# Optimization experiments

Measured on AMD Instinct MI355X. Metric: run time of the kernel, lower is better.

Reference implementation:

```python
import jax, jax.numpy as jnp
import numpy as np

B, S, HID = 1, 2048, 3584
NUM_HEADS, KV_HEADS, HEAD_DIM = 28, 4, 128
MROPE = [16, 24, 24]
HEAVY_RATIO, RECENT_RATIO, SINK, MIN_SEQ = 0.1, 0.1, 4, 1024
SCALING = HEAD_DIM ** -0.5
ROPE_THETA = 1000000.0


def rotate_half(x):
    h = x.shape[-1] // 2
    return jnp.concatenate([-x[..., h:], x[..., :h]], axis=-1)


def apply_mrope(q, k, cos, sin, mrope_section):
    # cos/sin: [3, B, S, head_dim]; interleave sections from the 3 position axes
    sec = mrope_section * 2
    splits = list(np.cumsum(sec)[:-1])
    cos_m = jnp.concatenate([m[i % 3] for i, m in enumerate(jnp.split(cos, splits, axis=-1))], axis=-1)[:, None]  # [B,1,S,D]
    sin_m = jnp.concatenate([m[i % 3] for i, m in enumerate(jnp.split(sin, splits, axis=-1))], axis=-1)[:, None]
    q_emb = q * cos_m + rotate_half(q) * sin_m
    k_emb = k * cos_m + rotate_half(k) * sin_m
    return q_emb, k_emb


def h2o_keep_mask(attn_weights, kv_len):
    # attn_weights: [B, H, Q, KV] post-softmax; accumulated score per head/key
    scores = attn_weights.sum(axis=(0, 2))  # [H, KV]
    heavy = max(1, int(HEAVY_RATIO * kv_len))
    recent = max(1, int(RECENT_RATIO * kv_len))
    keep = jnp.zeros((NUM_HEADS, kv_len), dtype=bool)
    ips = max(SINK * 2, int(0.2 * kv_len))  # image-protect prefix
    if kv_len > 3 * ips:
        keep = keep.at[:, :ips].set(True)
        ms = ips
    else:
        keep = keep.at[:, :SINK].set(True)
        ms = SINK
    keep = keep.at[:, kv_len - recent:].set(True)
    me = kv_len - recent
    k = min(heavy, me - ms)
    _, idx = jax.lax.top_k(scores[:, ms:me], k)  # [H, k]
    keep = keep.at[jnp.arange(NUM_HEADS)[:, None], idx + ms].set(True)
    return keep[None, :, None, :]  # [1, H, 1, KV]


def setup_inputs() -> dict:
    key = jax.random.key(0)
    ks = jax.random.split(key, 8)
    hidden_states = jax.random.normal(ks[0], (B, S, HID), jnp.float32)
    # additive causal mask
    causal = jnp.triu(jnp.full((S, S), -1e9, jnp.float32), k=1)
    attention_mask = causal[None, None]
    # mrope cos/sin (same positions on all 3 axes for text-only prefill)
    inv_freq = 1.0 / (ROPE_THETA ** (jnp.arange(0, HEAD_DIM, 2, dtype=jnp.float32) / HEAD_DIM))
    pos = jnp.arange(S, dtype=jnp.float32)
    freqs = pos[:, None] * inv_freq[None, :]            # [S, D/2]
    emb = jnp.concatenate([freqs, freqs], axis=-1)      # [S, D]
    cos = jnp.broadcast_to(jnp.cos(emb)[None, None], (3, B, S, HEAD_DIM))
    sin = jnp.broadcast_to(jnp.sin(emb)[None, None], (3, B, S, HEAD_DIM))
    sd = 0.02
    q_w = jax.random.normal(ks[1], (NUM_HEADS * HEAD_DIM, HID), jnp.float32) * sd
    q_b = jax.random.normal(ks[2], (NUM_HEADS * HEAD_DIM,), jnp.float32) * sd
    k_w = jax.random.normal(ks[3], (KV_HEADS * HEAD_DIM, HID), jnp.float32) * sd
    k_b = jax.random.normal(ks[4], (KV_HEADS * HEAD_DIM,), jnp.float32) * sd
    v_w = jax.random.normal(ks[5], (KV_HEADS * HEAD_DIM, HID), jnp.float32) * sd
    v_b = jax.random.normal(ks[6], (KV_HEADS * HEAD_DIM,), jnp.float32) * sd
    o_w = jax.random.normal(ks[7], (HID, NUM_HEADS * HEAD_DIM), jnp.float32) * sd
    return {"hidden_states": hidden_states, "attention_mask": attention_mask, "cos": cos, "sin": sin,
            "q_w": q_w, "q_b": q_b, "k_w": k_w, "k_b": k_b, "v_w": v_w, "v_b": v_b, "o_w": o_w}


def reference(hidden_states, attention_mask, cos, sin, q_w, q_b, k_w, k_b, v_w, v_b, o_w):
    b, s, _ = hidden_states.shape
    q = (hidden_states @ q_w.T + q_b).reshape(b, s, NUM_HEADS, HEAD_DIM).transpose(0, 2, 1, 3)
    k = (hidden_states @ k_w.T + k_b).reshape(b, s, KV_HEADS, HEAD_DIM).transpose(0, 2, 1, 3)
    v = (hidden_states @ v_w.T + v_b).reshape(b, s, KV_HEADS, HEAD_DIM).transpose(0, 2, 1, 3)
    q, k = apply_mrope(q, k, cos, sin, MROPE)
    n_rep = NUM_HEADS // KV_HEADS
    k = jnp.repeat(k, n_rep, axis=1)  # matches torch repeat_kv layout
    v = jnp.repeat(v, n_rep, axis=1)
    aw = jnp.einsum('bhqd,bhkd->bhqk', q, k) * SCALING + attention_mask
    aw = jax.nn.softmax(aw.astype(jnp.float32), axis=-1).astype(q.dtype)
    kv_len = s
    heavy = max(1, int(HEAVY_RATIO * kv_len))
    recent = max(1, int(RECENT_RATIO * kv_len))
    if kv_len >= MIN_SEQ and kv_len > SINK + recent + heavy:
        mask = h2o_keep_mask(jax.lax.stop_gradient(aw), kv_len)
        aw = aw * mask.astype(aw.dtype)
        aw = aw / jnp.clip(aw.sum(-1, keepdims=True), 1e-9)
    out = jnp.einsum('bhqk,bhkd->bhqd', aw, v)
    out = out.transpose(0, 2, 1, 3).reshape(b, s, NUM_HEADS * HEAD_DIM)
    return out @ o_w.T
```

## Files before the change

### kernel.cpp

```cpp
#include <hip/hip_runtime.h>
#include <hip/hip_bf16.h>
#include <stdint.h>

#define S_LEN 2048
#define HID 3584
#define NHEADS 28
#define KVHEADS 4
#define HD 128
#define QKV_N 4608
#define NREP 7
#define SCALE 0.08838834764831845f
#define NJOBS 896
#define NJOBS_LS 448

typedef __attribute__((ext_vector_type(8))) short bf16x8;
typedef __attribute__((ext_vector_type(8))) _Float16 f16x8;
typedef __attribute__((ext_vector_type(4))) float f32x4;

#define MFMA_B16(a, b, c) __builtin_amdgcn_mfma_f32_16x16x32_bf16((a), (b), (c), 0, 0, 0)
#define MFMA_F16(a, b, c) __builtin_amdgcn_mfma_f32_16x16x32_f16((a), (b), (c), 0, 0, 0)

__device__ __forceinline__ void gl_lds16(const void* g, void* l) {
  __builtin_amdgcn_global_load_lds(
      (__attribute__((address_space(1))) void*)(void*)(g),
      (__attribute__((address_space(3))) void*)(l), 16, 0, 0);
}

__global__ void cvt_f32_f16(const float* __restrict__ src, _Float16* __restrict__ dst, int n4) {
  int i = blockIdx.x * 256 + threadIdx.x;
  if (i >= n4) return;
  float4 v = ((const float4*)src)[i];
  _Float16 t[4] = {(_Float16)v.x, (_Float16)v.y, (_Float16)v.z, (_Float16)v.w};
  ((uint2*)dst)[i] = *(const uint2*)t;
}

template <bool HAS_BIAS>
__global__ __launch_bounds__(256, 4) void gemm_f16(
    const _Float16* __restrict__ A, int lda,
    const _Float16* __restrict__ B, int ldb,
    const float* __restrict__ bias, float* __restrict__ C, int ldc, int K) {
  __shared__ _Float16 lA[128 * 64], lB[128 * 64];
  const int tid = threadIdx.x;
  const int lane = tid & 63;
  const int wid = tid >> 6;
  const int wr = wid >> 1, wc = wid & 1;
  const int l15 = lane & 15, l4 = lane >> 4;
  const int bm = blockIdx.y * 128, bn = blockIdx.x * 128;
  f32x4 acc[4][4] = {};
  for (int k0 = 0; k0 < K; k0 += 64) {
    __syncthreads();
#pragma unroll
    for (int it = 0; it < 4; ++it) {
      int c = it * 256 + tid;
      int rw = c >> 3, sl = c & 7;
      int gcol = (sl ^ (rw & 7)) << 3;
      int lo = (it * 256 + (tid & 192)) * 8;
      gl_lds16(A + (size_t)(bm + rw) * lda + (k0 + gcol), &lA[lo]);
      gl_lds16(B + (size_t)(bn + rw) * ldb + (k0 + gcol), &lB[lo]);
    }
    __syncthreads();
#pragma unroll
    for (int kk = 0; kk < 2; ++kk) {
      f16x8 af[4], bf[4];
#pragma unroll
      for (int m = 0; m < 4; ++m) {
        int rA = wr * 64 + m * 16 + l15;
        af[m] = *(const f16x8*)&lA[rA * 64 + (((kk * 4 + l4) ^ (rA & 7)) << 3)];
      }
#pragma unroll
      for (int n = 0; n < 4; ++n) {
        int rB = wc * 64 + n * 16 + l15;
        bf[n] = *(const f16x8*)&lB[rB * 64 + (((kk * 4 + l4) ^ (rB & 7)) << 3)];
      }
#pragma unroll
      for (int m = 0; m < 4; ++m)
#pragma unroll
        for (int n = 0; n < 4; ++n)
          acc[m][n] = MFMA_F16(af[m], bf[n], acc[m][n]);
    }
  }
#pragma unroll
  for (int m = 0; m < 4; ++m)
#pragma unroll
    for (int n = 0; n < 4; ++n)
#pragma unroll
      for (int r = 0; r < 4; ++r) {
        size_t row = bm + wr * 64 + m * 16 + l4 * 4 + r;
        size_t col = bn + wc * 64 + n * 16 + l15;
        float v = acc[m][n][r];
        if (HAS_BIAS) v += bias[col];
        C[row * ldc + col] = v;
      }
}

__global__ void rope_f16(const float* __restrict__ qf, const float* __restrict__ cb,
                         const float* __restrict__ sb,
                         _Float16* __restrict__ q16, _Float16* __restrict__ k16) {
  int idx = blockIdx.x * 256 + threadIdx.x;
  int d1 = idx & 63;
  int hh = (idx >> 6) & 31;
  int s = idx >> 11;
  if (s >= S_LEN) return;
  const float* row = qf + (size_t)s * QKV_N + (hh < NHEADS ? hh * HD : HID + (hh - NHEADS) * HD);
  int d2 = d1 + 64;
  int ax1 = (d1 < 32) ? 0 : 1;
  int ax2 = (d2 < 80) ? 1 : 2;
  float c1 = cb[(size_t)ax1 * S_LEN * HD + (size_t)s * HD + d1];
  float s1 = sb[(size_t)ax1 * S_LEN * HD + (size_t)s * HD + d1];
  float c2 = cb[(size_t)ax2 * S_LEN * HD + (size_t)s * HD + d2];
  float s2 = sb[(size_t)ax2 * S_LEN * HD + (size_t)s * HD + d2];
  float x1 = row[d1], x2 = row[d2];
  float y1 = x1 * c1 - x2 * s1;
  float y2 = x2 * c2 + x1 * s2;
  _Float16* dp;
  size_t base;
  if (hh < NHEADS) { dp = q16; base = (size_t)s * HID + hh * HD; }
  else { dp = k16; base = (size_t)s * 512 + (hh - NHEADS) * HD; }
  dp[base + d1] = (_Float16)y1;
  dp[base + d2] = (_Float16)y2;
}

__global__ void vtrans(const float* __restrict__ qf, __hip_bfloat16* __restrict__ vt) {
  __shared__ __hip_bfloat16 t[64][65];
  const int j = blockIdx.z;
  const int d0 = blockIdx.y * 64;
  const int k0 = blockIdx.x * 64;
  const int tid = threadIdx.x;
#pragma unroll
  for (int half = 0; half < 2; ++half) {
    int r = half * 32 + (tid >> 3);
    int c = (tid & 7) * 8;
    const float* p = qf + (size_t)(k0 + r) * QKV_N + (HID + 512) + j * HD + d0 + c;
    float4 a = ((const float4*)p)[0];
    float4 b = ((const float4*)p)[1];
    t[c + 0][r] = __float2bfloat16(a.x); t[c + 1][r] = __float2bfloat16(a.y);
    t[c + 2][r] = __float2bfloat16(a.z); t[c + 3][r] = __float2bfloat16(a.w);
    t[c + 4][r] = __float2bfloat16(b.x); t[c + 5][r] = __float2bfloat16(b.y);
    t[c + 6][r] = __float2bfloat16(b.z); t[c + 7][r] = __float2bfloat16(b.w);
  }
  __syncthreads();
#pragma unroll
  for (int half = 0; half < 2; ++half) {
    int r = half * 32 + (tid >> 3);
    int c = (tid & 7) * 8;
    __hip_bfloat16 tmp[8];
#pragma unroll
    for (int u = 0; u < 8; ++u) tmp[u] = t[r][c + u];
    *(bf16x8*)&vt[(size_t)j * (HD * S_LEN) + (size_t)(d0 + r) * S_LEN + k0 + c] = *(const bf16x8*)tmp;
  }
}

template <typename T>
__device__ __forceinline__ void stageK_sw(T* dst, const T* gsrc, int ldg, int tid) {
#pragma unroll
  for (int it = 0; it < 4; ++it) {
    int c = it * 256 + tid;
    int rw = c >> 4, sl = c & 15;
    int gcol = (sl ^ (rw & 7)) << 3;
    gl_lds16(gsrc + (size_t)rw * ldg + gcol, dst + (size_t)(it * 256 + (tid & 192)) * 8);
  }
}
__device__ __forceinline__ void stageV_sw(__hip_bfloat16* dst, const __hip_bfloat16* gsrc,
                                          int ldg, int tid) {
#pragma unroll
  for (int it = 0; it < 4; ++it) {
    int c = it * 256 + tid;
    int rw = c >> 3, sl = c & 7;
    int gcol = (sl ^ (rw & 7)) << 3;
    gl_lds16(gsrc + (size_t)rw * ldg + gcol, dst + (size_t)(it * 256 + (tid & 192)) * 8);
  }
}

__global__ __launch_bounds__(256, 4) void attn_ls(
    const _Float16* __restrict__ q16, const _Float16* __restrict__ k16,
    float* __restrict__ scores, int* __restrict__ ctr) {
  __shared__ _Float16 Kh[2][64 * 128];
  __shared__ int sj;
  const int tid = threadIdx.x;
  const int lane = tid & 63, w = tid >> 6;
  const int l15 = lane & 15, l4 = lane >> 4;
  const int sw = l15 & 7;
  for (;;) {
    __syncthreads();
    if (tid == 0) sj = atomicAdd(ctr, 1);
    __syncthreads();
    const int j = sj;
    if (j >= NJOBS_LS) return;
    const int qb = 15 - j / 28, h = j % 28;
    const int hkv = h / NREP;
    const int nt = 2 * qb + 2;
    f16x8 qh[2][4];
#pragma unroll
    for (int f = 0; f < 2; ++f) {
      const _Float16* qp =
          q16 + (size_t)(qb * 128 + w * 32 + f * 16 + l15) * HID + h * HD + l4 * 8;
#pragma unroll
      for (int kk = 0; kk < 4; ++kk) qh[f][kk] = *(const f16x8*)(qp + kk * 32);
    }
    float lsum[2][4] = {};
    stageK_sw(Kh[0], k16 + hkv * HD, 512, tid);
    __syncthreads();
    for (int kt = 0; kt < nt; ++kt) {
      if (kt + 1 < nt)
        stageK_sw(Kh[(kt + 1) & 1], k16 + (size_t)((kt + 1) * 64) * 512 + hkv * HD, 512, tid);
      const _Float16* Kc = Kh[kt & 1];
      f32x4 acc[2][4] = {};
#pragma unroll
      for (int kk = 0; kk < 4; ++kk)
#pragma unroll
        for (int n = 0; n < 4; ++n) {
          f16x8 bh = *(const f16x8*)&Kc[(n * 16 + l15) * 128 + (((kk * 4 + l4) ^ sw) << 3)];
#pragma unroll
          for (int f = 0; f < 2; ++f) acc[f][n] = MFMA_F16(qh[f][kk], bh, acc[f][n]);
        }
      const bool tail = (kt >= 2 * qb);
#pragma unroll
      for (int f = 0; f < 2; ++f)
#pragma unroll
        for (int r = 0; r < 4; ++r) {
          int rowg = qb * 128 + w * 32 + f * 16 + l4 * 4 + r;
#pragma unroll
          for (int n = 0; n < 4; ++n)
            if (!tail || (kt * 64 + n * 16 + l15) <= rowg)
              lsum[f][r] += __expf(acc[f][n][r] * SCALE);
        }
      __syncthreads();
    }
    float invl[2][4];
#pragma unroll
    for (int f = 0; f < 2; ++f)
#pragma unroll
      for (int r = 0; r < 4; ++r) {
        float s = lsum[f][r];
        s += __shfl_xor(s, 1);
        s += __shfl_xor(s, 2);
        s += __shfl_xor(s, 4);
        s += __shfl_xor(s, 8);
        invl[f][r] = 1.0f / s;
      }
    stageK_sw(Kh[0], k16 + hkv * HD, 512, tid);
    __syncthreads();
    for (int kt = 0; kt < nt; ++kt) {
      if (kt + 1 < nt)
        stageK_sw(Kh[(kt + 1) & 1], k16 + (size_t)((kt + 1) * 64) * 512 + hkv * HD, 512, tid);
      const _Float16* Kc = Kh[kt & 1];
      f32x4 acc[2][4] = {};
#pragma unroll
      for (int kk = 0; kk < 4; ++kk)
#pragma unroll
        for (int n = 0; n < 4; ++n) {
          f16x8 bh = *(const f16x8*)&Kc[(n * 16 + l15) * 128 + (((kk * 4 + l4) ^ sw) << 3)];
#pragma unroll
          for (int f = 0; f < 2; ++f) acc[f][n] = MFMA_F16(qh[f][kk], bh, acc[f][n]);
        }
      const bool tail = (kt >= 2 * qb);
      float colsum[4] = {0.f, 0.f, 0.f, 0.f};
#pragma unroll
      for (int f = 0; f < 2; ++f)
#pragma unroll
        for (int r = 0; r < 4; ++r) {
          int rowg = qb * 128 + w * 32 + f * 16 + l4 * 4 + r;
#pragma unroll
          for (int n = 0; n < 4; ++n)
            if (!tail || (kt * 64 + n * 16 + l15) <= rowg)
              colsum[n] += __expf(acc[f][n][r] * SCALE) * invl[f][r];
        }
#pragma unroll
      for (int n = 0; n < 4; ++n) {
        colsum[n] += __shfl_xor(colsum[n], 16);
        colsum[n] += __shfl_xor(colsum[n], 32);
      }
      if (lane < 16) {
#pragma unroll
        for (int n = 0; n < 4; ++n)
          atomicAdd(&scores[h * S_LEN + kt * 64 + n * 16 + lane], colsum[n]);
      }
      __syncthreads();
    }
  }
}

__global__ void h2o_topk(const float* __restrict__ scores, unsigned char* __restrict__ keep) {
  const int h = blockIdx.x;
  const int tid = threadIdx.x;
  const int MS = 409, ME = 1844, REGN = 1435, KSEL = 204;
  __shared__ float sv[1435];
  __shared__ int cnt, eqn;
  __shared__ int eqlist[256];
  for (int i = tid; i < REGN; i += 256) sv[i] = scores[h * S_LEN + MS + i];
  for (int i = tid; i < S_LEN; i += 256)
    keep[h * S_LEN + i] = (i < MS || i >= ME) ? 1 : 0;
  __syncthreads();
  unsigned lo = 0u, hi = 0x7f800000u;
  while (hi - lo > 1u) {
    unsigned mid = lo + ((hi - lo) >> 1);
    if (tid == 0) cnt = 0;
    __syncthreads();
    int lc = 0;
    for (int i = tid; i < REGN; i += 256) lc += (__float_as_uint(sv[i]) >= mid) ? 1 : 0;
    if (lc) atomicAdd(&cnt, lc);
    __syncthreads();
    int c = cnt;
    __syncthreads();
    if (c >= KSEL) lo = mid;
    else hi = mid;
  }
  if (tid == 0) { cnt = 0; eqn = 0; }
  __syncthreads();
  int lgt = 0;
  for (int i = tid; i < REGN; i += 256) {
    unsigned b = __float_as_uint(sv[i]);
    if (b > lo) { keep[h * S_LEN + MS + i] = 1; lgt++; }
    else if (b == lo) {
      int p = atomicAdd(&eqn, 1);
      if (p < 256) eqlist[p] = i;
    }
  }
  if (lgt) atomicAdd(&cnt, lgt);
  __syncthreads();
  if (tid == 0) {
    int r = KSEL - cnt;
    int ne = eqn > 256 ? 256 : eqn;
    for (int t = 0; t < r; ++t) {
      int best = 0x7fffffff, bj = -1;
      for (int j = 0; j < ne; ++j)
        if (eqlist[j] < best) { best = eqlist[j]; bj = j; }
      if (bj < 0) break;
      keep[h * S_LEN + MS + best] = 1;
      eqlist[bj] = 0x7fffffff;
    }
  }
}

__global__ __launch_bounds__(256, 2) void attn_out(
    const _Float16* __restrict__ q16, const _Float16* __restrict__ k16,
    const __hip_bfloat16* __restrict__ vt, const unsigned char* __restrict__ keep,
    _Float16* __restrict__ ctx, int* __restrict__ ctr) {
  __shared__ _Float16 Kh[2][64 * 128];
  __shared__ __hip_bfloat16 Vtl[2][128 * 64];
  __shared__ __hip_bfloat16 Wt[4][16 * 64];
  __shared__ int sj;
  const int tid = threadIdx.x;
  const int lane = tid & 63, w = tid >> 6;
  const int l15 = lane & 15, l4 = lane >> 4;
  const int sw = l15 & 7;
  for (;;) {
    __syncthreads();
    if (tid == 0) sj = atomicAdd(ctr, 1);
    __syncthreads();
    const int j = sj;
    if (j >= NJOBS) return;
    const int qb = 31 - j / 28, h = j % 28;
    const int hkv = h / NREP;
    const int nt = qb + 1;
    f16x8 qh[4];
    {
      const _Float16* qp = q16 + (size_t)(qb * 64 + w * 16 + l15) * HID + h * HD + l4 * 8;
#pragma unroll
      for (int kk = 0; kk < 4; ++kk) qh[kk] = *(const f16x8*)(qp + kk * 32);
    }
    f32x4 o[8] = {};
    float dens[4] = {0.f, 0.f, 0.f, 0.f};
    stageK_sw(Kh[0], k16 + hkv * HD, 512, tid);
    stageV_sw(Vtl[0], vt + (size_t)hkv * (HD * S_LEN), S_LEN, tid);
    __syncthreads();
    for (int kt = 0; kt < nt; ++kt) {
      if (kt + 1 < nt) {
        stageK_sw(Kh[(kt + 1) & 1], k16 + (size_t)((kt + 1) * 64) * 512 + hkv * HD, 512, tid);
        stageV_sw(Vtl[(kt + 1) & 1], vt + (size_t)hkv * (HD * S_LEN) + (kt + 1) * 64, S_LEN, tid);
      }
      const _Float16* Kc = Kh[kt & 1];
      const __hip_bfloat16* Vc = Vtl[kt & 1];
      f32x4 acc[4] = {};
#pragma unroll
      for (int kk = 0; kk < 4; ++kk)
#pragma unroll
        for (int n = 0; n < 4; ++n) {
          f16x8 bh = *(const f16x8*)&Kc[(n * 16 + l15) * 128 + (((kk * 4 + l4) ^ sw) << 3)];
          acc[n] = MFMA_F16(qh[kk], bh, acc[n]);
        }
      const bool diag = (kt == qb);
      float kf[4];
#pragma unroll
      for (int n = 0; n < 4; ++n)
        kf[n] = (float)keep[h * S_LEN + kt * 64 + n * 16 + l15];
#pragma unroll
      for (int r = 0; r < 4; ++r) {
        int rowg = qb * 64 + w * 16 + l4 * 4 + r;
        int row16 = l4 * 4 + r;
#pragma unroll
        for (int n = 0; n < 4; ++n) {
          int coll = n * 16 + l15;
          float wv = 0.f;
          if (!diag || (kt * 64 + coll) <= rowg)
            wv = kf[n] * __expf(acc[n][r] * SCALE);
          dens[r] += wv;
          Wt[w][row16 * 64 + (coll ^ ((row16 & 7) << 3))] = __float2bfloat16(wv);
        }
      }
#pragma unroll
      for (int kk = 0; kk < 2; ++kk) {
        bf16x8 af = *(const bf16x8*)&Wt[w][l15 * 64 + ((kk * 32 + l4 * 8) ^ (sw << 3))];
#pragma unroll
        for (int n = 0; n < 8; ++n) {
          bf16x8 bf = *(const bf16x8*)&Vc[(n * 16 + l15) * 64 + (((kk * 4 + l4) ^ sw) << 3)];
          o[n] = MFMA_B16(af, bf, o[n]);
        }
      }
      __syncthreads();
    }
    float invd[4];
#pragma unroll
    for (int r = 0; r < 4; ++r) {
      float d = dens[r];
      d += __shfl_xor(d, 1);
      d += __shfl_xor(d, 2);
      d += __shfl_xor(d, 4);
      d += __shfl_xor(d, 8);
      invd[r] = 1.0f / fmaxf(d, 1e-30f);
    }
#pragma unroll
    for (int n = 0; n < 8; ++n)
#pragma unroll
      for (int r = 0; r < 4; ++r) {
        size_t row = qb * 64 + w * 16 + l4 * 4 + r;
        size_t col = h * HD + n * 16 + l15;
        ctx[row * HID + col] = (_Float16)(o[n][r] * invd[r]);
      }
  }
}

extern "C" void kernel_launch(void* const* d_in, const int* in_sizes, int n_in,
                              void* d_out, int out_size, void* d_ws, size_t ws_size,
                              hipStream_t stream) {
  const float* hidden = (const float*)d_in[0];
  const float* cosb = (const float*)d_in[2];
  const float* sinb = (const float*)d_in[3];
  const float* q_w = (const float*)d_in[4];
  const float* q_b = (const float*)d_in[5];
  const float* k_w = (const float*)d_in[6];
  const float* k_b = (const float*)d_in[7];
  const float* v_w = (const float*)d_in[8];
  const float* v_b = (const float*)d_in[9];
  const float* o_w = (const float*)d_in[10];

  char* ws = (char*)d_ws;
  float* qkv_f32 = (float*)(ws + 0);
  _Float16* hf16 = (_Float16*)(ws + 37748736);
  _Float16* wqkv16 = (_Float16*)(ws + 52428800);
  float* biasb = (float*)(ws + 85458944);
  _Float16* q16 = (_Float16*)(ws + 37748736);
  _Float16* wo16 = (_Float16*)(ws + 52428800);
  _Float16* k16 = (_Float16*)(ws + 85477376);
  __hip_bfloat16* vt = (__hip_bfloat16*)(ws + 87574528);
  float* scores = (float*)(ws + 89671680);
  unsigned char* keep = (unsigned char*)(ws + 89901056);
  int* ctrs = (int*)(ws + 89958400);
  _Float16* ctx16 = (_Float16*)(ws + 0);

  hipMemcpyAsync(biasb, q_b, 3584 * 4, hipMemcpyDeviceToDevice, stream);
  hipMemcpyAsync(biasb + 3584, k_b, 512 * 4, hipMemcpyDeviceToDevice, stream);
  hipMemcpyAsync(biasb + 4096, v_b, 512 * 4, hipMemcpyDeviceToDevice, stream);

  cvt_f32_f16<<<7168, 256, 0, stream>>>(hidden, hf16, 1835008);
  cvt_f32_f16<<<12544, 256, 0, stream>>>(q_w, wqkv16, 3211264);
  cvt_f32_f16<<<1792, 256, 0, stream>>>(k_w, wqkv16 + (size_t)3584 * 3584, 458752);
  cvt_f32_f16<<<1792, 256, 0, stream>>>(v_w, wqkv16 + (size_t)4096 * 3584, 458752);

  gemm_f16<true><<<dim3(36, 16), 256, 0, stream>>>(hf16, HID, wqkv16, HID,
                                                   biasb, qkv_f32, QKV_N, HID);

  cvt_f32_f16<<<12544, 256, 0, stream>>>(o_w, wo16, 3211264);

  rope_f16<<<16384, 256, 0, stream>>>(qkv_f32, cosb, sinb, q16, k16);
  vtrans<<<dim3(32, 2, 4), 256, 0, stream>>>(qkv_f32, vt);
  hipMemsetAsync(scores, 0, NHEADS * S_LEN * 4, stream);
  hipMemsetAsync(ctrs, 0, 8, stream);

  attn_ls<<<512, 256, 0, stream>>>(q16, k16, scores, &ctrs[0]);
  h2o_topk<<<28, 256, 0, stream>>>(scores, keep);
  attn_out<<<512, 256, 0, stream>>>(q16, k16, vt, keep, ctx16, &ctrs[1]);

  gemm_f16<false><<<dim3(28, 16), 256, 0, stream>>>(ctx16, HID, wo16, HID,
                                                    nullptr, (float*)d_out, HID, HID);
}
```

Baseline: 455.6 us.

## Split H2O score kernel into key-chunked row-sum and column-score passes

The single persistent attn_ls kernel, which computed softmax row sums and then column scores per (query block, head) job, is replaced by two grid-launched kernels. Each splits the key range into chunks of up to eight 64-key tiles, giving 1120 blocks in place of 448 jobs. Row sums are combined with atomics into a new lbuf buffer, and a masking branch is hoisted so full tiles skip the causal check. This aims at better load balance and occupancy for long causal rows, at the cost of an extra launch, more atomics and reloading Q per chunk.

```diff
diff --git a/kernel.cpp b/kernel.cpp
--- a/kernel.cpp
+++ b/kernel.cpp
@@ -11,7 +11,7 @@
 #define NREP 7
 #define SCALE 0.08838834764831845f
 #define NJOBS 896
-#define NJOBS_LS 448
+#define NJOBS_KC 1120
 
 typedef __attribute__((ext_vector_type(8))) short bf16x8;
 typedef __attribute__((ext_vector_type(8))) _Float16 f16x8;
@@ -24,6 +24,13 @@
   __builtin_amdgcn_global_load_lds(
       (__attribute__((address_space(1))) void*)(void*)(g),
       (__attribute__((address_space(3))) void*)(l), 16, 0, 0);
+}
+
+__device__ __forceinline__ void decode_qc(int t, int& qb, int& ck) {
+  if (t < 4) { qb = t; ck = 0; }
+  else if (t < 12) { qb = 4 + ((t - 4) >> 1); ck = (t - 4) & 1; }
+  else if (t < 24) { qb = 8 + (t - 12) / 3; ck = (t - 12) % 3; }
+  else { qb = 12 + ((t - 24) >> 2); ck = (t - 24) & 3; }
 }
 
 __global__ void cvt_f32_f16(const float* __restrict__ src, _Float16* __restrict__ dst, int n4) {
@@ -171,49 +178,55 @@
   }
 }
 
-__global__ __launch_bounds__(256, 4) void attn_ls(
+__global__ __launch_bounds__(256, 4) void attn_l(
     const _Float16* __restrict__ q16, const _Float16* __restrict__ k16,
-    float* __restrict__ scores, int* __restrict__ ctr) {
+    float* __restrict__ lbuf) {
   __shared__ _Float16 Kh[2][64 * 128];
-  __shared__ int sj;
+  const int j = blockIdx.x;
+  const int h = j % 28;
+  int qb, ck;
+  decode_qc(j / 28, qb, ck);
+  const int hkv = h / NREP;
+  const int nt = 2 * qb + 2;
+  const int kt0 = ck * 8;
+  const int kt1 = (kt0 + 8 < nt) ? kt0 + 8 : nt;
   const int tid = threadIdx.x;
   const int lane = tid & 63, w = tid >> 6;
   const int l15 = lane & 15, l4 = lane >> 4;
   const int sw = l15 & 7;
-  for (;;) {
-    __syncthreads();
-    if (tid == 0) sj = atomicAdd(ctr, 1);
-    __syncthreads();
-    const int j = sj;
-    if (j >= NJOBS_LS) return;
-    const int qb = 15 - j / 28, h = j % 28;
-    const int hkv = h / NREP;
-    const int nt = 2 * qb + 2;
-    f16x8 qh[2][4];
-#pragma unroll
-    for (int f = 0; f < 2; ++f) {
-      const _Float16* qp =
-          q16 + (size_t)(qb * 128 + w * 32 + f * 16 + l15) * HID + h * HD + l4 * 8;
-#pragma unroll
-      for (int kk = 0; kk < 4; ++kk) qh[f][kk] = *(const f16x8*)(qp + kk * 32);
-    }
-    float lsum[2][4] = {};
-    stageK_sw(Kh[0], k16 + hkv * HD, 512, tid);
-    __syncthreads();
-    for (int kt = 0; kt < nt; ++kt) {
-      if (kt + 1 < nt)
-        stageK_sw(Kh[(kt + 1) & 1], k16 + (size_t)((kt + 1) * 64) * 512 + hkv * HD, 512, tid);
-      const _Float16* Kc = Kh[kt & 1];
-      f32x4 acc[2][4] = {};
-#pragma unroll
-      for (int kk = 0; kk < 4; ++kk)
-#pragma unroll
-        for (int n = 0; n < 4; ++n) {
-          f16x8 bh = *(const f16x8*)&Kc[(n * 16 + l15) * 128 + (((kk * 4 + l4) ^ sw) << 3)];
-#pragma unroll
-          for (int f = 0; f < 2; ++f) acc[f][n] = MFMA_F16(qh[f][kk], bh, acc[f][n]);
-        }
-      const bool tail = (kt >= 2 * qb);
+  f16x8 qh[2][4];
+#pragma unroll
+  for (int f = 0; f < 2; ++f) {
+    const _Float16* qp =
+        q16 + (size_t)(qb * 128 + w * 32 + f * 16 + l15) * HID + h * HD + l4 * 8;
+#pragma unroll
+    for (int kk = 0; kk < 4; ++kk) qh[f][kk] = *(const f16x8*)(qp + kk * 32);
+  }
+  float lsum[2][4] = {};
+  stageK_sw(Kh[0], k16 + (size_t)(kt0 * 64) * 512 + hkv * HD, 512, tid);
+  __syncthreads();
+  for (int kt = kt0; kt < kt1; ++kt) {
+    if (kt + 1 < kt1)
+      stageK_sw(Kh[(kt + 1) & 1], k16 + (size_t)((kt + 1) * 64) * 512 + hkv * HD, 512, tid);
+    const _Float16* Kc = Kh[kt & 1];
+    f32x4 acc[2][4] = {};
+#pragma unroll
+    for (int kk = 0; kk < 4; ++kk)
+#pragma unroll
+      for (int n = 0; n < 4; ++n) {
+        f16x8 bh = *(const f16x8*)&Kc[(n * 16 + l15) * 128 + (((kk * 4 + l4) ^ sw) << 3)];
+#pragma unroll
+        for (int f = 0; f < 2; ++f) acc[f][n] = MFMA_F16(qh[f][kk], bh, acc[f][n]);
+      }
+    if (kt < 2 * qb) {
+#pragma unroll
+      for (int f = 0; f < 2; ++f)
+#pragma unroll
+        for (int r = 0; r < 4; ++r)
+#pragma unroll
+          for (int n = 0; n < 4; ++n)
+            lsum[f][r] += __expf(acc[f][n][r] * SCALE);
+    } else {
 #pragma unroll
       for (int f = 0; f < 2; ++f)
 #pragma unroll
@@ -221,40 +234,81 @@
           int rowg = qb * 128 + w * 32 + f * 16 + l4 * 4 + r;
 #pragma unroll
           for (int n = 0; n < 4; ++n)
-            if (!tail || (kt * 64 + n * 16 + l15) <= rowg)
+            if ((kt * 64 + n * 16 + l15) <= rowg)
               lsum[f][r] += __expf(acc[f][n][r] * SCALE);
         }
-      __syncthreads();
-    }
-    float invl[2][4];
-#pragma unroll
-    for (int f = 0; f < 2; ++f)
-#pragma unroll
-      for (int r = 0; r < 4; ++r) {
-        float s = lsum[f][r];
-        s += __shfl_xor(s, 1);
-        s += __shfl_xor(s, 2);
-        s += __shfl_xor(s, 4);
-        s += __shfl_xor(s, 8);
-        invl[f][r] = 1.0f / s;
-      }
-    stageK_sw(Kh[0], k16 + hkv * HD, 512, tid);
-    __syncthreads();
-    for (int kt = 0; kt < nt; ++kt) {
-      if (kt + 1 < nt)
-        stageK_sw(Kh[(kt + 1) & 1], k16 + (size_t)((kt + 1) * 64) * 512 + hkv * HD, 512, tid);
-      const _Float16* Kc = Kh[kt & 1];
-      f32x4 acc[2][4] = {};
-#pragma unroll
-      for (int kk = 0; kk < 4; ++kk)
-#pragma unroll
-        for (int n = 0; n < 4; ++n) {
-          f16x8 bh = *(const f16x8*)&Kc[(n * 16 + l15) * 128 + (((kk * 4 + l4) ^ sw) << 3)];
-#pragma unroll
-          for (int f = 0; f < 2; ++f) acc[f][n] = MFMA_F16(qh[f][kk], bh, acc[f][n]);
-        }
-      const bool tail = (kt >= 2 * qb);
-      float colsum[4] = {0.f, 0.f, 0.f, 0.f};
+    }
+    __syncthreads();
+  }
+#pragma unroll
+  for (int f = 0; f < 2; ++f)
+#pragma unroll
+    for (int r = 0; r < 4; ++r) {
+      float s = lsum[f][r];
+      s += __shfl_xor(s, 1);
+      s += __shfl_xor(s, 2);
+      s += __shfl_xor(s, 4);
+      s += __shfl_xor(s, 8);
+      if (l15 == 0)
+        atomicAdd(&lbuf[h * S_LEN + qb * 128 + w * 32 + f * 16 + l4 * 4 + r], s);
+    }
+}
+
+__global__ __launch_bounds__(256, 4) void attn_sc(
+    const _Float16* __restrict__ q16, const _Float16* __restrict__ k16,
+    const float* __restrict__ lbuf, float* __restrict__ scores) {
+  __shared__ _Float16 Kh[2][64 * 128];
+  const int j = blockIdx.x;
+  const int h = j % 28;
+  int qb, ck;
+  decode_qc(j / 28, qb, ck);
+  const int hkv = h / NREP;
+  const int nt = 2 * qb + 2;
+  const int kt0 = ck * 8;
+  const int kt1 = (kt0 + 8 < nt) ? kt0 + 8 : nt;
+  const int tid = threadIdx.x;
+  const int lane = tid & 63, w = tid >> 6;
+  const int l15 = lane & 15, l4 = lane >> 4;
+  const int sw = l15 & 7;
+  f16x8 qh[2][4];
+#pragma unroll
+  for (int f = 0; f < 2; ++f) {
+    const _Float16* qp =
+        q16 + (size_t)(qb * 128 + w * 32 + f * 16 + l15) * HID + h * HD + l4 * 8;
+#pragma unroll
+    for (int kk = 0; kk < 4; ++kk) qh[f][kk] = *(const f16x8*)(qp + kk * 32);
+  }
+  float invl[2][4];
+#pragma unroll
+  for (int f = 0; f < 2; ++f)
+#pragma unroll
+    for (int r = 0; r < 4; ++r)
+      invl[f][r] = 1.0f / lbuf[h * S_LEN + qb * 128 + w * 32 + f * 16 + l4 * 4 + r];
+  stageK_sw(Kh[0], k16 + (size_t)(kt0 * 64) * 512 + hkv * HD, 512, tid);
+  __syncthreads();
+  for (int kt = kt0; kt < kt1; ++kt) {
+    if (kt + 1 < kt1)
+      stageK_sw(Kh[(kt + 1) & 1], k16 + (size_t)((kt + 1) * 64) * 512 + hkv * HD, 512, tid);
+    const _Float16* Kc = Kh[kt & 1];
+    f32x4 acc[2][4] = {};
+#pragma unroll
+    for (int kk = 0; kk < 4; ++kk)
+#pragma unroll
+      for (int n = 0; n < 4; ++n) {
+        f16x8 bh = *(const f16x8*)&Kc[(n * 16 + l15) * 128 + (((kk * 4 + l4) ^ sw) << 3)];
+#pragma unroll
+        for (int f = 0; f < 2; ++f) acc[f][n] = MFMA_F16(qh[f][kk], bh, acc[f][n]);
+      }
+    float colsum[4] = {0.f, 0.f, 0.f, 0.f};
+    if (kt < 2 * qb) {
+#pragma unroll
+      for (int f = 0; f < 2; ++f)
+#pragma unroll
+        for (int r = 0; r < 4; ++r)
+#pragma unroll
+          for (int n = 0; n < 4; ++n)
+            colsum[n] += __expf(acc[f][n][r] * SCALE) * invl[f][r];
+    } else {
 #pragma unroll
       for (int f = 0; f < 2; ++f)
 #pragma unroll
@@ -262,21 +316,21 @@
           int rowg = qb * 128 + w * 32 + f * 16 + l4 * 4 + r;
 #pragma unroll
           for (int n = 0; n < 4; ++n)
-            if (!tail || (kt * 64 + n * 16 + l15) <= rowg)
+            if ((kt * 64 + n * 16 + l15) <= rowg)
               colsum[n] += __expf(acc[f][n][r] * SCALE) * invl[f][r];
         }
-#pragma unroll
-      for (int n = 0; n < 4; ++n) {
-        colsum[n] += __shfl_xor(colsum[n], 16);
-        colsum[n] += __shfl_xor(colsum[n], 32);
-      }
-      if (lane < 16) {
-#pragma unroll
-        for (int n = 0; n < 4; ++n)
-          atomicAdd(&scores[h * S_LEN + kt * 64 + n * 16 + lane], colsum[n]);
-      }
-      __syncthreads();
-    }
+    }
+#pragma unroll
+    for (int n = 0; n < 4; ++n) {
+      colsum[n] += __shfl_xor(colsum[n], 16);
+      colsum[n] += __shfl_xor(colsum[n], 32);
+    }
+    if (lane < 16) {
+#pragma unroll
+      for (int n = 0; n < 4; ++n)
+        atomicAdd(&scores[h * S_LEN + kt * 64 + n * 16 + lane], colsum[n]);
+    }
+    __syncthreads();
   }
 }
 
@@ -456,6 +510,7 @@
   float* scores = (float*)(ws + 89671680);
   unsigned char* keep = (unsigned char*)(ws + 89901056);
   int* ctrs = (int*)(ws + 89958400);
+  float* lbuf = (float*)(ws + 89958464);
   _Float16* ctx16 = (_Float16*)(ws + 0);
 
   hipMemcpyAsync(biasb, q_b, 3584 * 4, hipMemcpyDeviceToDevice, stream);
@@ -475,9 +530,11 @@
   rope_f16<<<16384, 256, 0, stream>>>(qkv_f32, cosb, sinb, q16, k16);
   vtrans<<<dim3(32, 2, 4), 256, 0, stream>>>(qkv_f32, vt);
   hipMemsetAsync(scores, 0, NHEADS * S_LEN * 4, stream);
-  hipMemsetAsync(ctrs, 0, 8, stream);
-
-  attn_ls<<<512, 256, 0, stream>>>(q16, k16, scores, &ctrs[0]);
+  hipMemsetAsync(lbuf, 0, NHEADS * S_LEN * 4, stream);
+  hipMemsetAsync(ctrs, 0, 64, stream);
+
+  attn_l<<<NJOBS_KC, 256, 0, stream>>>(q16, k16, lbuf);
+  attn_sc<<<NJOBS_KC, 256, 0, stream>>>(q16, k16, lbuf, scores);
   h2o_topk<<<28, 256, 0, stream>>>(scores, keep);
   attn_out<<<512, 256, 0, stream>>>(q16, k16, vt, keep, ctx16, &ctrs[1]);
 
```

After: 420.5 us. -7.7%, faster.
